# Kernel optimization log

Hardware: AMD Instinct MI355X
Metric: run time of the kernel (lower is better)

The kernel has to match this reference:

```python
import jax, jax.numpy as jnp
import numpy as np

B = 5                      # dat_sz hardcoded in module; kernel shapes force batch == 5
X_DIM = 4096
H_DIM = 4096
T_DIM = 4096
D_DIM = X_DIM // T_DIM     # = 1 (required so z_dim == t_dim broadcasts in reparameterize_nm)
L_DIM = D_DIM * (D_DIM + 1) // 2
Z_DIM = T_DIM * L_DIM      # = 4096


def _linear_params(key, din, dout):
    kw, kb = jax.random.split(key)
    W = jax.random.normal(kw, (din, dout), dtype=jnp.float32) / np.float32(np.sqrt(din))
    b = jax.random.normal(kb, (dout,), dtype=jnp.float32) * np.float32(0.01)
    return W, b


def setup_inputs() -> dict:
    key = jax.random.key(0)
    ks = jax.random.split(key, 20)
    inp = {}
    inp["x"] = jax.random.normal(ks[0], (B, X_DIM), dtype=jnp.float32)
    inp["eps_xi"] = jax.random.normal(ks[1], (B, T_DIM), dtype=jnp.float32)
    inp["eps_f"] = jax.random.normal(ks[2], (B, D_DIM), dtype=jnp.float32)
    inp["eps_z"] = jax.random.normal(ks[3], (B, Z_DIM), dtype=jnp.float32)
    inp["W1"], inp["b1"] = _linear_params(ks[4], X_DIM, H_DIM)
    inp["W11"], inp["b11"] = _linear_params(ks[5], H_DIM, T_DIM)
    inp["W12"], inp["b12"] = _linear_params(ks[6], H_DIM, T_DIM)
    inp["W2"], inp["b2"] = _linear_params(ks[7], D_DIM, H_DIM)
    inp["W21"], inp["b21"] = _linear_params(ks[8], H_DIM, Z_DIM)
    inp["W22"], inp["b22"] = _linear_params(ks[9], H_DIM, T_DIM)
    inp["W23"], inp["b23"] = _linear_params(ks[10], X_DIM + Z_DIM, H_DIM)
    inp["W24"], inp["b24"] = _linear_params(ks[11], H_DIM, T_DIM + D_DIM)
    inp["W25"], inp["b25"] = _linear_params(ks[12], H_DIM, T_DIM + D_DIM)
    inp["W3"], inp["b3"] = _linear_params(ks[13], Z_DIM, H_DIM)
    inp["W31"], inp["b31"] = _linear_params(ks[14], H_DIM, X_DIM)
    inp["W32"], inp["b32"] = _linear_params(ks[15], H_DIM, X_DIM)
    inp["s"] = jax.random.normal(ks[16], (B, T_DIM), dtype=jnp.float32)
    inp["t"] = jax.random.normal(ks[17], (B, D_DIM), dtype=jnp.float32)
    inp["sigma"] = jnp.asarray(0.01, dtype=jnp.float32)
    inp["w"] = jnp.ones((T_DIM,), dtype=jnp.float32) / np.float32(T_DIM)
    inp["dist"] = 1  # unused by forward (matches torch signature)
    return inp


def _ard_kernel(a, b, sigma, w):
    # K[i,j] = sigma^2 * exp(-0.5 * sum_d w_d (a_i,d - b_j,d)^2)
    # Vectorized replacement of the original O(B^2) Python double loop.
    d2 = (a[:, None, :] - b[None, :, :]) ** 2            # [B, B, T]
    return (sigma ** 2) * jnp.exp(-0.5 * jnp.einsum('ijt,t->ij', d2, w))


def reference(x, eps_xi, eps_f, eps_z,
              W1, b1, W11, b11, W12, b12,
              W2, b2, W21, b21, W22, b22,
              W23, b23, W24, b24, W25, b25,
              W3, b3, W31, b31, W32, b32,
              s, t, sigma, w, dist):
    relu = jax.nn.relu
    # encode_1
    h1 = relu(x @ W1 + b1)
    qxi_mean = h1 @ W11 + b11
    log_qxi_cov = h1 @ W12 + b12
    # reparameterize_nm
    xi = jnp.exp(0.5 * log_qxi_cov) * eps_xi + qxi_mean
    # reparameterize_gp (training branch)
    K_ss = _ard_kernel(s, s, sigma, w)                    # [5,5]
    K_xs = _ard_kernel(xi, s, sigma, w)                   # [5,5]
    kk_inv = K_xs @ jnp.linalg.inv(K_ss)                  # [5,5]
    qf_mean = kk_inv @ t                                  # [5,D]
    cov = _ard_kernel(xi, xi, sigma, w) - kk_inv @ _ard_kernel(s, xi, sigma, w)
    qf_cov = jnp.diag(cov)                                # [5]
    f = jnp.sqrt(qf_cov)[:, None] * eps_f + qf_mean       # [5,D]
    # encode_2
    h2 = relu(f @ W2 + b2)
    z_mean = h2 @ W21 + b21                               # [5,Z]
    z_cov = h2 @ W22 + b22                                # [5,T] (== Z since d_dim=1)
    z = jnp.exp(0.5 * z_cov) * eps_z + z_mean
    # encode_3
    h23 = relu(jnp.concatenate([x, z], axis=1) @ W23 + b23)
    r_mean = h23 @ W24 + b24                              # [5,T+D]
    r_cov = h23 @ W25 + b25
    # decode
    h3 = relu(z @ W3 + b3)
    x_mean = h3 @ W31 + b31
    x_cov = h3 @ W32 + b32
    # losses
    qf_cov2 = jnp.broadcast_to(qf_cov[:, None], (B, D_DIM))
    q_mean = jnp.concatenate([qxi_mean, qf_mean], axis=1)
    q_cov = jnp.concatenate([log_qxi_cov, jnp.log(qf_cov2)], axis=1)
    kld1 = 0.5 * jnp.sum(-z_cov - 1.0 + jnp.exp(z_cov) + z_mean ** 2) / B
    kld2 = 0.5 * jnp.sum(r_cov - q_cov - 1.0
                         + jnp.exp(q_cov - r_cov)
                         + (q_mean - r_mean) ** 2 * jnp.exp(-r_cov)) / B
    kld_loss = kld1 + kld2
    log_pi = jnp.log(jnp.asarray(np.pi, dtype=jnp.float32))
    nll_loss = 0.5 * jnp.sum(log_pi + x_cov + jnp.exp(-x_cov) * (x - x_mean) ** 2) / B
    return (kld_loss, nll_loss, z_mean, z_cov, x_mean, x_cov)
```

## Files before the change

kernel.cpp:

```cpp
#include <hip/hip_runtime.h>
#include <math.h>

#define B5 5
#define DX 4096
#define DT 4096
#define DR 4097

enum {
  WS_SUMS  = 0,
  WS_CNT1  = 3,
  WS_CNT2  = 4,
  WS_ZERO_END = 8,
  WS_ACT1  = 16,
  WS_ACT23 = WS_ACT1  + 20480,
  WS_ACT3  = WS_ACT23 + 20480,
  WS_QXI_F = WS_ACT3  + 20480,
  WS_LQC_F = WS_QXI_F + 20480,
  WS_XIV   = WS_LQC_F + 20480,
  WS_Z     = WS_XIV   + 20480,
  WS_KSS   = WS_Z     + 20480,
  WS_KXS   = WS_KSS + 32,
  WS_F     = WS_KXS + 32,
  WS_QFM   = WS_F   + 8,
  WS_QFC   = WS_QFM + 8,
  WS_PART  = 143472,
  WS_P_H1  = WS_PART,
  WS_P_QXI = WS_P_H1  + 1310720,
  WS_P_LQC = WS_P_QXI + 1310720,
  WS_P_ZM  = WS_P_LQC + 1310720,
  WS_P_ZC  = WS_P_ZM  + 1310720,
  WS_P_H23 = WS_P_ZC  + 1310720,
  WS_P_H3  = WS_P_H23 + 2621440,
  WS_P_RM  = WS_P_H3  + 1310720,
  WS_P_RC  = WS_P_RM  + 1311040,
  WS_P_XM  = WS_P_RC  + 1311040,
  WS_P_XC  = WS_P_XM  + 1310720,
  WS_END   = WS_P_XC  + 1310720
};

#define GCOLS 128
#define GK    64
#define WROWS 16

__device__ inline float wave_sum(float v) {
  #pragma unroll
  for (int o = 32; o > 0; o >>= 1) v += __shfl_down(v, o, 64);
  return v;
}

template<int PROLOG, int DUAL, int ALIGNED>
__device__ __forceinline__ void gemm5_body(
    float* sx, float* red, int bx, int by,
    const float* __restrict__ p0, const float* __restrict__ p1,
    const float* __restrict__ p2,
    const float* __restrict__ Wa, const float* __restrict__ Wb,
    float* __restrict__ Pa,       float* __restrict__ Pb,
    int din, int dout)
{
  const int tid  = threadIdx.x;
  const int lane = tid & 63;
  const int wv   = tid >> 6;
  const long i0  = (long)by * GK;
  const long r0  = i0 + (long)wv * WROWS;

  float* sw = sx + wv * 80;
  for (int t = lane; t < B5 * WROWS; t += 64) {
    int b  = t >> 4;
    int il = t & 15;
    int i  = (int)(r0 + il);
    float v;
    if (PROLOG == 0)      v = p0[(long)b * din + i];
    else if (PROLOG == 2) v = fmaxf(p0[b] * p1[i] + p2[i], 0.f);
    else                  v = (i < DX) ? p0[(long)b * DX + i] : p1[(long)b * DT + (i - DX)];
    sw[t] = v;
  }

  const long o0 = (long)bx * GCOLS + lane * 2;
  const bool v0 = (o0 < dout);
  const bool v1 = (o0 + 1 < dout);

  float accA[B5][2] = {};
  float accB[B5][2] = {};
  const float* wa = Wa + r0 * dout + o0;
  const float* wb = DUAL ? (Wb + r0 * dout + o0) : nullptr;

  #pragma unroll 8
  for (int il = 0; il < WROWS; ++il) {
    float w0a, w1a, w0b = 0.f, w1b = 0.f;
    if (ALIGNED) {
      float2 ta = *(const float2*)wa; w0a = ta.x; w1a = ta.y;
      if (DUAL) { float2 tb = *(const float2*)wb; w0b = tb.x; w1b = tb.y; }
    } else {
      w0a = v0 ? wa[0] : 0.f; w1a = v1 ? wa[1] : 0.f;
      if (DUAL) { w0b = v0 ? wb[0] : 0.f; w1b = v1 ? wb[1] : 0.f; }
    }
    #pragma unroll
    for (int b = 0; b < B5; ++b) {
      float xv = sw[b * WROWS + il];
      accA[b][0] += xv * w0a; accA[b][1] += xv * w1a;
      if (DUAL) { accB[b][0] += xv * w0b; accB[b][1] += xv * w1b; }
    }
    wa += dout; if (DUAL) wb += dout;
  }

  const int NJ = DUAL ? 20 : 10;
  if (wv > 0) {
    float* rr = red + (long)(wv - 1) * NJ * 64 + lane;
    #pragma unroll
    for (int b = 0; b < B5; ++b) {
      rr[(b*2)*64] = accA[b][0]; rr[(b*2+1)*64] = accA[b][1];
      if (DUAL) { rr[(10+b*2)*64] = accB[b][0]; rr[(10+b*2+1)*64] = accB[b][1]; }
    }
  }
  __syncthreads();
  if (wv == 0) {
    #pragma unroll
    for (int w2 = 0; w2 < 3; ++w2) {
      const float* rr = red + (long)w2 * NJ * 64 + lane;
      #pragma unroll
      for (int b = 0; b < B5; ++b) {
        accA[b][0] += rr[(b*2)*64]; accA[b][1] += rr[(b*2+1)*64];
        if (DUAL) { accB[b][0] += rr[(10+b*2)*64]; accB[b][1] += rr[(10+b*2+1)*64]; }
      }
    }
    if (v0) {
      #pragma unroll
      for (int b = 0; b < B5; ++b) {
        float* pa = Pa + ((long)by * B5 + b) * dout + o0;
        if (ALIGNED) *(float2*)pa = make_float2(accA[b][0], accA[b][1]);
        else { pa[0] = accA[b][0]; if (v1) pa[1] = accA[b][1]; }
        if (DUAL) {
          float* pb = Pb + ((long)by * B5 + b) * dout + o0;
          if (ALIGNED) *(float2*)pb = make_float2(accB[b][0], accB[b][1]);
          else { pb[0] = accB[b][0]; if (v1) pb[1] = accB[b][1]; }
        }
      }
    }
  }
}

template<int PROLOG, int DUAL, int ALIGNED>
__global__ __launch_bounds__(256) void gemm5(
    const float* __restrict__ p0, const float* __restrict__ p1,
    const float* __restrict__ p2,
    const float* __restrict__ Wa, const float* __restrict__ Wb,
    float* __restrict__ Pa,       float* __restrict__ Pb,
    int din, int dout)
{
  __shared__ float sx[4 * 80];
  __shared__ float red[3 * 20 * 64];
  gemm5_body<PROLOG, DUAL, ALIGNED>(sx, red, blockIdx.x, blockIdx.y,
      p0, p1, p2, Wa, Wb, Pa, Pb, din, dout);
}

__global__ __launch_bounds__(256) void gemm5_G46(
    const float* __restrict__ x,   const float* __restrict__ z,
    const float* __restrict__ W23, float* __restrict__ P23,
    const float* __restrict__ W3,  float* __restrict__ P3)
{
  __shared__ float sx[4 * 80];
  __shared__ float red[3 * 20 * 64];
  int id = blockIdx.x;
  if (id < 4096) {
    gemm5_body<3, 0, 1>(sx, red, id & 31, id >> 5, x, z, nullptr,
                        W23, nullptr, P23, nullptr, 8192, 4096);
  } else {
    id -= 4096;
    gemm5_body<0, 0, 1>(sx, red, id & 31, id >> 5, z, nullptr, nullptr,
                        W3, nullptr, P3, nullptr, 4096, 4096);
  }
}

__global__ __launch_bounds__(256) void gemm5_G57(
    const float* __restrict__ act23,
    const float* __restrict__ W24, const float* __restrict__ W25,
    float* __restrict__ PRM,       float* __restrict__ PRC,
    const float* __restrict__ act3,
    const float* __restrict__ W31, const float* __restrict__ W32,
    float* __restrict__ PXM,       float* __restrict__ PXC)
{
  __shared__ float sx[4 * 80];
  __shared__ float red[3 * 20 * 64];
  int id = blockIdx.x;
  if (id < 2112) {
    gemm5_body<0, 1, 0>(sx, red, id % 33, id / 33, act23, nullptr, nullptr,
                        W24, W25, PRM, PRC, 4096, 4097);
  } else {
    id -= 2112;
    gemm5_body<0, 1, 1>(sx, red, id & 31, id >> 5, act3, nullptr, nullptr,
                        W31, W32, PXM, PXC, 4096, 4096);
  }
}

__global__ __launch_bounds__(256) void k_act1(
    const float* __restrict__ P, const float* __restrict__ bias, float* __restrict__ act,
    float* __restrict__ ctrl)
{
  if (blockIdx.x == 0 && threadIdx.x < WS_ZERO_END) ctrl[threadIdx.x] = 0.f;
  int idx = blockIdx.x * 256 + threadIdx.x;
  int b = idx >> 12, col = idx & (DT - 1);
  const float* pp = P + (long)b * DT + col;
  float s = 0.f;
  #pragma unroll 8
  for (int ks = 0; ks < 64; ++ks) s += pp[(long)ks * (B5 * DT)];
  act[idx] = fmaxf(s + bias[col], 0.f);
}

__global__ __launch_bounds__(256) void k_act23(
    const float* __restrict__ P23, const float* __restrict__ b23, float* __restrict__ act23,
    const float* __restrict__ P3,  const float* __restrict__ b3,  float* __restrict__ act3)
{
  int idx = blockIdx.x * 256 + threadIdx.x;
  if (idx < B5 * DT) {
    int b = idx >> 12, col = idx & (DT - 1);
    const float* pp = P23 + (long)b * DT + col;
    float s = 0.f;
    #pragma unroll 8
    for (int ks = 0; ks < 128; ++ks) s += pp[(long)ks * (B5 * DT)];
    act23[idx] = fmaxf(s + b23[col], 0.f);
  } else {
    int j = idx - B5 * DT;
    int b = j >> 12, col = j & (DT - 1);
    const float* pp = P3 + (long)b * DT + col;
    float s = 0.f;
    #pragma unroll 8
    for (int ks = 0; ks < 64; ++ks) s += pp[(long)ks * (B5 * DT)];
    act3[j] = fmaxf(s + b3[col], 0.f);
  }
}

__global__ __launch_bounds__(256) void k_xi(
    const float* __restrict__ Pq, const float* __restrict__ Pl,
    const float* __restrict__ b11, const float* __restrict__ b12,
    const float* __restrict__ eps_xi,
    float* __restrict__ qf, float* __restrict__ lf, float* __restrict__ xiv)
{
  int idx = blockIdx.x * 256 + threadIdx.x;
  if (idx >= B5 * DT) return;
  int b = idx >> 12, col = idx & (DT - 1);
  const float* pq = Pq + (long)b * DT + col;
  const float* pl = Pl + (long)b * DT + col;
  float sq = 0.f, sl = 0.f;
  #pragma unroll 8
  for (int ks = 0; ks < 64; ++ks) { sq += pq[(long)ks * (B5 * DT)]; sl += pl[(long)ks * (B5 * DT)]; }
  float qm = sq + b11[col];
  float lq = sl + b12[col];
  qf[idx] = qm; lf[idx] = lq;
  xiv[idx] = expf(0.5f * lq) * eps_xi[idx] + qm;
}

__global__ __launch_bounds__(256) void k_ardgp(
    const float* __restrict__ s,    const float* __restrict__ xiv,
    const float* __restrict__ w,    const float* __restrict__ sigma,
    const float* __restrict__ t_in, const float* __restrict__ eps_f,
    float* __restrict__ Kss, float* __restrict__ Kxs, int* __restrict__ cnt,
    float* __restrict__ fv, float* __restrict__ qfm, float* __restrict__ qfc)
{
  const int bid = blockIdx.x;
  const bool xs = (bid >= 25);
  int q = xs ? bid - 25 : bid;
  const int i = q / 5, j = q % 5;
  const float* aa = xs ? (xiv + (long)i * DT) : (s + (long)i * DT);
  const float* bb = s + (long)j * DT;

  float sum = 0.f;
  for (int t = threadIdx.x; t < DT; t += 256) {
    float d = aa[t] - bb[t];
    sum += w[t] * d * d;
  }
  sum = wave_sum(sum);
  __shared__ float red[4];
  int lane = threadIdx.x & 63, wv = threadIdx.x >> 6;
  if (lane == 0) red[wv] = sum;
  __syncthreads();

  if (threadIdx.x == 0) {
    float tot = red[0] + red[1] + red[2] + red[3];
    float sg = sigma[0];
    float K = sg * sg * expf(-0.5f * tot);
    (xs ? Kxs : Kss)[i * 5 + j] = K;
    __threadfence();
    int old = atomicAdd(cnt, 1);
    if (old == 49) {
      __threadfence();
      double M[5][5], Inv[5][5];
      for (int a = 0; a < 5; ++a)
        for (int b = 0; b < 5; ++b) { M[a][b] = Kss[a * 5 + b]; Inv[a][b] = (a == b) ? 1.0 : 0.0; }
      for (int c = 0; c < 5; ++c) {
        int p = c; double best = fabs(M[c][c]);
        for (int r = c + 1; r < 5; ++r) if (fabs(M[r][c]) > best) { best = fabs(M[r][c]); p = r; }
        if (p != c)
          for (int k = 0; k < 5; ++k) {
            double tm = M[c][k]; M[c][k] = M[p][k]; M[p][k] = tm;
            tm = Inv[c][k]; Inv[c][k] = Inv[p][k]; Inv[p][k] = tm;
          }
        double piv = 1.0 / M[c][c];
        for (int k = 0; k < 5; ++k) { M[c][k] *= piv; Inv[c][k] *= piv; }
        for (int r = 0; r < 5; ++r) if (r != c) {
          double m = M[r][c];
          for (int k = 0; k < 5; ++k) { M[r][k] -= m * M[c][k]; Inv[r][k] -= m * Inv[c][k]; }
        }
      }
      double kk[5][5];
      for (int a = 0; a < 5; ++a)
        for (int b = 0; b < 5; ++b) {
          double acc = 0.0;
          for (int k = 0; k < 5; ++k) acc += (double)Kxs[a * 5 + k] * Inv[k][b];
          kk[a][b] = acc;
        }
      double sg2 = (double)sg * (double)sg;
      for (int a = 0; a < 5; ++a) {
        double qm = 0.0, qc = sg2;
        for (int b = 0; b < 5; ++b) { qm += kk[a][b] * (double)t_in[b]; qc -= kk[a][b] * (double)Kxs[a * 5 + b]; }
        if (qc < 1e-12) qc = 1e-12;
        qfm[a] = (float)qm;
        qfc[a] = (float)qc;
        fv[a]  = sqrtf((float)qc) * eps_f[a] + (float)qm;
      }
    }
  }
}

__global__ __launch_bounds__(256) void k_z(
    const float* __restrict__ Pm, const float* __restrict__ Pc,
    const float* __restrict__ b21, const float* __restrict__ b22,
    const float* __restrict__ eps_z,
    float* __restrict__ out_zm, float* __restrict__ out_zc,
    float* __restrict__ zv, float* __restrict__ kld1sum)
{
  int idx = blockIdx.x * 256 + threadIdx.x;
  float term = 0.f;
  if (idx < B5 * DT) {
    int b = idx >> 12, col = idx & (DT - 1);
    const float* pm = Pm + (long)b * DT + col;
    const float* pc = Pc + (long)b * DT + col;
    float sm = 0.f, sc = 0.f;
    #pragma unroll 8
    for (int ks = 0; ks < 64; ++ks) { sm += pm[(long)ks * (B5 * DT)]; sc += pc[(long)ks * (B5 * DT)]; }
    float zm = sm + b21[col];
    float zc = sc + b22[col];
    out_zm[idx] = zm; out_zc[idx] = zc;
    zv[idx] = expf(0.5f * zc) * eps_z[idx] + zm;
    term = -zc - 1.f + expf(zc) + zm * zm;
  }
  term = wave_sum(term);
  if ((threadIdx.x & 63) == 0) atomicAdd(kld1sum, term);
}

__global__ __launch_bounds__(256) void k_fin(
    const float* __restrict__ Prm, const float* __restrict__ Prc,
    const float* __restrict__ b24, const float* __restrict__ b25,
    const float* __restrict__ qxi, const float* __restrict__ lqc,
    const float* __restrict__ qfm, const float* __restrict__ qfc,
    const float* __restrict__ Pxm, const float* __restrict__ Pxc,
    const float* __restrict__ b31, const float* __restrict__ b32,
    const float* __restrict__ x,
    float* __restrict__ out_xm, float* __restrict__ out_xc,
    float* __restrict__ sums, int* __restrict__ cnt, float* __restrict__ out01)
{
  const int gtid = blockIdx.x * 256 + threadIdx.x;
  float t2 = 0.f, t3 = 0.f;
  if (gtid < B5 * DR) {
    int b = gtid / DR, col = gtid % DR;
    const float* pm = Prm + (long)b * DR + col;
    const float* pc = Prc + (long)b * DR + col;
    float sm = 0.f, sc = 0.f;
    #pragma unroll 8
    for (int ks = 0; ks < 64; ++ks) { sm += pm[(long)ks * (B5 * DR)]; sc += pc[(long)ks * (B5 * DR)]; }
    float rm = sm + b24[col];
    float rc = sc + b25[col];
    float qm, qc;
    if (col < DT) { qm = qxi[(long)b * DT + col]; qc = lqc[(long)b * DT + col]; }
    else          { qm = qfm[b]; qc = logf(qfc[b]); }
    float d = qm - rm;
    t2 = rc - qc - 1.f + expf(qc - rc) + d * d * expf(-rc);
  } else {
    int idx = gtid - B5 * DR;
    if (idx < B5 * DX) {
      int b = idx >> 12, col = idx & (DX - 1);
      const float* pm = Pxm + (long)b * DX + col;
      const float* pc = Pxc + (long)b * DX + col;
      float sm = 0.f, sc = 0.f;
      #pragma unroll 8
      for (int ks = 0; ks < 64; ++ks) { sm += pm[(long)ks * (B5 * DX)]; sc += pc[(long)ks * (B5 * DX)]; }
      float xm = sm + b31[col];
      float xc = sc + b32[col];
      out_xm[idx] = xm; out_xc[idx] = xc;
      float d = x[idx] - xm;
      t3 = 1.14472988584940017f + xc + expf(-xc) * d * d;
    }
  }
  t2 = wave_sum(t2);
  t3 = wave_sum(t3);
  if ((threadIdx.x & 63) == 0) {
    if (t2 != 0.f) atomicAdd(&sums[1], t2);
    if (t3 != 0.f) atomicAdd(&sums[2], t3);
  }
  __syncthreads();
  if (threadIdx.x == 0) {
    __threadfence();
    int old = atomicAdd(cnt, 1);
    if (old == (int)gridDim.x - 1) {
      __threadfence();
      out01[0] = 0.5f * (sums[0] + sums[1]) / (float)B5;
      out01[1] = 0.5f * sums[2] / (float)B5;
    }
  }
}

extern "C" void kernel_launch(void* const* d_in, const int* in_sizes, int n_in,
                              void* d_out, int out_size, void* d_ws, size_t ws_size,
                              hipStream_t stream)
{
  const float* x      = (const float*)d_in[0];
  const float* eps_xi = (const float*)d_in[1];
  const float* eps_f  = (const float*)d_in[2];
  const float* eps_z  = (const float*)d_in[3];
  const float* W1  = (const float*)d_in[4];  const float* b1  = (const float*)d_in[5];
  const float* W11 = (const float*)d_in[6];  const float* b11 = (const float*)d_in[7];
  const float* W12 = (const float*)d_in[8];  const float* b12 = (const float*)d_in[9];
  const float* W2  = (const float*)d_in[10]; const float* b2  = (const float*)d_in[11];
  const float* W21 = (const float*)d_in[12]; const float* b21 = (const float*)d_in[13];
  const float* W22 = (const float*)d_in[14]; const float* b22 = (const float*)d_in[15];
  const float* W23 = (const float*)d_in[16]; const float* b23 = (const float*)d_in[17];
  const float* W24 = (const float*)d_in[18]; const float* b24 = (const float*)d_in[19];
  const float* W25 = (const float*)d_in[20]; const float* b25 = (const float*)d_in[21];
  const float* W3  = (const float*)d_in[22]; const float* b3  = (const float*)d_in[23];
  const float* W31 = (const float*)d_in[24]; const float* b31 = (const float*)d_in[25];
  const float* W32 = (const float*)d_in[26]; const float* b32 = (const float*)d_in[27];
  const float* s     = (const float*)d_in[28];
  const float* t     = (const float*)d_in[29];
  const float* sigma = (const float*)d_in[30];
  const float* w     = (const float*)d_in[31];

  float* ws  = (float*)d_ws;
  float* out = (float*)d_out;

  dim3 blk(256);

  gemm5<0,0,1><<<dim3(32,64), blk, 0, stream>>>(
      x, nullptr, nullptr, W1, nullptr, ws + WS_P_H1, nullptr, 4096, 4096);
  k_act1<<<80, blk, 0, stream>>>(ws + WS_P_H1, b1, ws + WS_ACT1, ws);
  gemm5<0,1,1><<<dim3(32,64), blk, 0, stream>>>(
      ws + WS_ACT1, nullptr, nullptr, W11, W12, ws + WS_P_QXI, ws + WS_P_LQC, 4096, 4096);
  k_xi<<<80, blk, 0, stream>>>(
      ws + WS_P_QXI, ws + WS_P_LQC, b11, b12, eps_xi,
      ws + WS_QXI_F, ws + WS_LQC_F, ws + WS_XIV);
  k_ardgp<<<50, blk, 0, stream>>>(
      s, ws + WS_XIV, w, sigma, t, eps_f,
      ws + WS_KSS, ws + WS_KXS, (int*)(ws + WS_CNT1),
      ws + WS_F, ws + WS_QFM, ws + WS_QFC);
  gemm5<2,1,1><<<dim3(32,64), blk, 0, stream>>>(
      ws + WS_F, W2, b2, W21, W22, ws + WS_P_ZM, ws + WS_P_ZC, 4096, 4096);
  k_z<<<80, blk, 0, stream>>>(
      ws + WS_P_ZM, ws + WS_P_ZC, b21, b22, eps_z,
      out + 2, out + 2 + 20480, ws + WS_Z, ws + WS_SUMS);
  gemm5_G46<<<6144, blk, 0, stream>>>(
      x, ws + WS_Z, W23, ws + WS_P_H23, W3, ws + WS_P_H3);
  k_act23<<<160, blk, 0, stream>>>(
      ws + WS_P_H23, b23, ws + WS_ACT23, ws + WS_P_H3, b3, ws + WS_ACT3);
  gemm5_G57<<<4160, blk, 0, stream>>>(
      ws + WS_ACT23, W24, W25, ws + WS_P_RM, ws + WS_P_RC,
      ws + WS_ACT3,  W31, W32, ws + WS_P_XM, ws + WS_P_XC);
  k_fin<<<161, blk, 0, stream>>>(
      ws + WS_P_RM, ws + WS_P_RC, b24, b25,
      ws + WS_QXI_F, ws + WS_LQC_F,
      ws + WS_QFM, ws + WS_QFC,
      ws + WS_P_XM, ws + WS_P_XC, b31, b32, x,
      out + 2 + 40960, out + 2 + 61440,
      ws + WS_SUMS, (int*)(ws + WS_CNT2), out);
}
```

Baseline: 242.0 us.

## Split-K partial reductions across 8 warps per block and fuse xi with ARD kernel

```diff
diff --git a/kernel.cpp b/kernel.cpp
--- a/kernel.cpp
+++ b/kernel.cpp
@@ -5,11 +5,14 @@
 #define DX 4096
 #define DT 4096
 #define DR 4097
+#define PSZ 20480
+#define PSZR 20485
 
 enum {
   WS_SUMS  = 0,
-  WS_CNT1  = 3,
-  WS_CNT2  = 4,
+  WS_CNT_XI  = 3,
+  WS_CNT_FIN = 4,
+  WS_CNT_ARD = 5,
   WS_ZERO_END = 8,
   WS_ACT1  = 16,
   WS_ACT23 = WS_ACT1  + 20480,
@@ -48,6 +51,26 @@
   return v;
 }
 
+template<int PER>
+__device__ __forceinline__ float red_block(
+    const float* __restrict__ P, long psz, long e, int tid, float* r)
+{
+  int j = tid >> 5;
+  const float* pp = P + (long)j * PER * psz + e;
+  float s = 0.f;
+  #pragma unroll
+  for (int k = 0; k < PER; ++k) s += pp[(long)k * psz];
+  r[tid] = s;
+  __syncthreads();
+  float tot = 0.f;
+  if (tid < 32) {
+    #pragma unroll
+    for (int jj = 0; jj < 8; ++jj) tot += r[jj * 32 + tid];
+  }
+  __syncthreads();
+  return tot;
+}
+
 template<int PROLOG, int DUAL, int ALIGNED>
 __device__ __forceinline__ void gemm5_body(
     float* sx, float* red, int bx, int by,
@@ -197,90 +220,101 @@
     float* __restrict__ ctrl)
 {
   if (blockIdx.x == 0 && threadIdx.x < WS_ZERO_END) ctrl[threadIdx.x] = 0.f;
-  int idx = blockIdx.x * 256 + threadIdx.x;
-  int b = idx >> 12, col = idx & (DT - 1);
-  const float* pp = P + (long)b * DT + col;
-  float s = 0.f;
-  #pragma unroll 8
-  for (int ks = 0; ks < 64; ++ks) s += pp[(long)ks * (B5 * DT)];
-  act[idx] = fmaxf(s + bias[col], 0.f);
+  __shared__ float r[256];
+  int tid = threadIdx.x;
+  long e = (long)blockIdx.x * 32 + (tid & 31);
+  float s = red_block<8>(P, PSZ, e, tid, r);
+  if (tid < 32) {
+    int col = (int)(e & 4095);
+    act[e] = fmaxf(s + bias[col], 0.f);
+  }
 }
 
 __global__ __launch_bounds__(256) void k_act23(
     const float* __restrict__ P23, const float* __restrict__ b23, float* __restrict__ act23,
     const float* __restrict__ P3,  const float* __restrict__ b3,  float* __restrict__ act3)
 {
-  int idx = blockIdx.x * 256 + threadIdx.x;
-  if (idx < B5 * DT) {
-    int b = idx >> 12, col = idx & (DT - 1);
-    const float* pp = P23 + (long)b * DT + col;
-    float s = 0.f;
-    #pragma unroll 8
-    for (int ks = 0; ks < 128; ++ks) s += pp[(long)ks * (B5 * DT)];
-    act23[idx] = fmaxf(s + b23[col], 0.f);
+  __shared__ float r[256];
+  int tid = threadIdx.x;
+  if (blockIdx.x < 640) {
+    long e = (long)blockIdx.x * 32 + (tid & 31);
+    float s = red_block<16>(P23, PSZ, e, tid, r);
+    if (tid < 32) {
+      int col = (int)(e & 4095);
+      act23[e] = fmaxf(s + b23[col], 0.f);
+    }
   } else {
-    int j = idx - B5 * DT;
-    int b = j >> 12, col = j & (DT - 1);
-    const float* pp = P3 + (long)b * DT + col;
-    float s = 0.f;
-    #pragma unroll 8
-    for (int ks = 0; ks < 64; ++ks) s += pp[(long)ks * (B5 * DT)];
-    act3[j] = fmaxf(s + b3[col], 0.f);
-  }
-}
-
-__global__ __launch_bounds__(256) void k_xi(
+    long e = (long)(blockIdx.x - 640) * 32 + (tid & 31);
+    float s = red_block<8>(P3, PSZ, e, tid, r);
+    if (tid < 32) {
+      int col = (int)(e & 4095);
+      act3[e] = fmaxf(s + b3[col], 0.f);
+    }
+  }
+}
+
+__global__ __launch_bounds__(256) void k_xiard(
     const float* __restrict__ Pq, const float* __restrict__ Pl,
     const float* __restrict__ b11, const float* __restrict__ b12,
     const float* __restrict__ eps_xi,
-    float* __restrict__ qf, float* __restrict__ lf, float* __restrict__ xiv)
-{
-  int idx = blockIdx.x * 256 + threadIdx.x;
-  if (idx >= B5 * DT) return;
-  int b = idx >> 12, col = idx & (DT - 1);
-  const float* pq = Pq + (long)b * DT + col;
-  const float* pl = Pl + (long)b * DT + col;
-  float sq = 0.f, sl = 0.f;
-  #pragma unroll 8
-  for (int ks = 0; ks < 64; ++ks) { sq += pq[(long)ks * (B5 * DT)]; sl += pl[(long)ks * (B5 * DT)]; }
-  float qm = sq + b11[col];
-  float lq = sl + b12[col];
-  qf[idx] = qm; lf[idx] = lq;
-  xiv[idx] = expf(0.5f * lq) * eps_xi[idx] + qm;
-}
-
-__global__ __launch_bounds__(256) void k_ardgp(
-    const float* __restrict__ s,    const float* __restrict__ xiv,
-    const float* __restrict__ w,    const float* __restrict__ sigma,
+    const float* __restrict__ s,   const float* __restrict__ w,
+    const float* __restrict__ sigma,
     const float* __restrict__ t_in, const float* __restrict__ eps_f,
-    float* __restrict__ Kss, float* __restrict__ Kxs, int* __restrict__ cnt,
+    float* __restrict__ qf, float* __restrict__ lf, float* __restrict__ xiv,
+    float* __restrict__ Kss, float* __restrict__ Kxs,
+    int* __restrict__ cnt_xi, int* __restrict__ cnt_ard,
     float* __restrict__ fv, float* __restrict__ qfm, float* __restrict__ qfc)
 {
-  const int bid = blockIdx.x;
+  __shared__ float r[256];
+  int tid = threadIdx.x;
+  if (blockIdx.x < 640) {
+    long e = (long)blockIdx.x * 32 + (tid & 31);
+    float sq = red_block<8>(Pq, PSZ, e, tid, r);
+    float sl = red_block<8>(Pl, PSZ, e, tid, r);
+    if (tid < 32) {
+      int col = (int)(e & 4095);
+      float qm = sq + b11[col];
+      float lq = sl + b12[col];
+      qf[e] = qm; lf[e] = lq;
+      xiv[e] = expf(0.5f * lq) * eps_xi[e] + qm;
+    }
+    __threadfence();
+    __syncthreads();
+    if (tid == 0) atomicAdd(cnt_xi, 1);
+    return;
+  }
+
+  const int bid = blockIdx.x - 640;
   const bool xs = (bid >= 25);
   int q = xs ? bid - 25 : bid;
   const int i = q / 5, j = q % 5;
+
+  if (xs) {
+    if (tid == 0) { while (atomicAdd(cnt_xi, 0) < 640) {} }
+    __syncthreads();
+    __threadfence();
+  }
   const float* aa = xs ? (xiv + (long)i * DT) : (s + (long)i * DT);
   const float* bb = s + (long)j * DT;
 
   float sum = 0.f;
-  for (int t = threadIdx.x; t < DT; t += 256) {
+  for (int t = tid; t < DT; t += 256) {
     float d = aa[t] - bb[t];
     sum += w[t] * d * d;
   }
   sum = wave_sum(sum);
-  __shared__ float red[4];
-  int lane = threadIdx.x & 63, wv = threadIdx.x >> 6;
-  if (lane == 0) red[wv] = sum;
+  __shared__ float red4[4];
+  int lane = tid & 63, wv = tid >> 6;
+  if (lane == 0) red4[wv] = sum;
   __syncthreads();
 
-  if (threadIdx.x == 0) {
-    float tot = red[0] + red[1] + red[2] + red[3];
+  if (tid == 0) {
+    float tot = red4[0] + red4[1] + red4[2] + red4[3];
     float sg = sigma[0];
     float K = sg * sg * expf(-0.5f * tot);
     (xs ? Kxs : Kss)[i * 5 + j] = K;
     __threadfence();
-    int old = atomicAdd(cnt, 1);
+    int old = atomicAdd(cnt_ard, 1);
     if (old == 49) {
       __threadfence();
       double M[5][5], Inv[5][5];
@@ -288,7 +322,7 @@
         for (int b = 0; b < 5; ++b) { M[a][b] = Kss[a * 5 + b]; Inv[a][b] = (a == b) ? 1.0 : 0.0; }
       for (int c = 0; c < 5; ++c) {
         int p = c; double best = fabs(M[c][c]);
-        for (int r = c + 1; r < 5; ++r) if (fabs(M[r][c]) > best) { best = fabs(M[r][c]); p = r; }
+        for (int rr = c + 1; rr < 5; ++rr) if (fabs(M[rr][c]) > best) { best = fabs(M[rr][c]); p = rr; }
         if (p != c)
           for (int k = 0; k < 5; ++k) {
             double tm = M[c][k]; M[c][k] = M[p][k]; M[p][k] = tm;
@@ -296,9 +330,9 @@
           }
         double piv = 1.0 / M[c][c];
         for (int k = 0; k < 5; ++k) { M[c][k] *= piv; Inv[c][k] *= piv; }
-        for (int r = 0; r < 5; ++r) if (r != c) {
-          double m = M[r][c];
-          for (int k = 0; k < 5; ++k) { M[r][k] -= m * M[c][k]; Inv[r][k] -= m * Inv[c][k]; }
+        for (int rr = 0; rr < 5; ++rr) if (rr != c) {
+          double m = M[rr][c];
+          for (int k = 0; k < 5; ++k) { M[rr][k] -= m * M[c][k]; Inv[rr][k] -= m * Inv[c][k]; }
         }
       }
       double kk[5][5];
@@ -328,23 +362,24 @@
     float* __restrict__ out_zm, float* __restrict__ out_zc,
     float* __restrict__ zv, float* __restrict__ kld1sum)
 {
-  int idx = blockIdx.x * 256 + threadIdx.x;
+  __shared__ float r[256];
+  int tid = threadIdx.x;
+  long e = (long)blockIdx.x * 32 + (tid & 31);
+  float sm = red_block<8>(Pm, PSZ, e, tid, r);
+  float sc = red_block<8>(Pc, PSZ, e, tid, r);
   float term = 0.f;
-  if (idx < B5 * DT) {
-    int b = idx >> 12, col = idx & (DT - 1);
-    const float* pm = Pm + (long)b * DT + col;
-    const float* pc = Pc + (long)b * DT + col;
-    float sm = 0.f, sc = 0.f;
-    #pragma unroll 8
-    for (int ks = 0; ks < 64; ++ks) { sm += pm[(long)ks * (B5 * DT)]; sc += pc[(long)ks * (B5 * DT)]; }
+  if (tid < 32) {
+    int col = (int)(e & 4095);
     float zm = sm + b21[col];
     float zc = sc + b22[col];
-    out_zm[idx] = zm; out_zc[idx] = zc;
-    zv[idx] = expf(0.5f * zc) * eps_z[idx] + zm;
+    out_zm[e] = zm; out_zc[e] = zc;
+    zv[e] = expf(0.5f * zc) * eps_z[e] + zm;
     term = -zc - 1.f + expf(zc) + zm * zm;
   }
-  term = wave_sum(term);
-  if ((threadIdx.x & 63) == 0) atomicAdd(kld1sum, term);
+  if (tid < 64) {
+    term = wave_sum(term);
+    if (tid == 0 && term != 0.f) atomicAdd(kld1sum, term);
+  }
 }
 
 __global__ __launch_bounds__(256) void k_fin(
@@ -358,46 +393,49 @@
     float* __restrict__ out_xm, float* __restrict__ out_xc,
     float* __restrict__ sums, int* __restrict__ cnt, float* __restrict__ out01)
 {
-  const int gtid = blockIdx.x * 256 + threadIdx.x;
-  float t2 = 0.f, t3 = 0.f;
-  if (gtid < B5 * DR) {
-    int b = gtid / DR, col = gtid % DR;
-    const float* pm = Prm + (long)b * DR + col;
-    const float* pc = Prc + (long)b * DR + col;
-    float sm = 0.f, sc = 0.f;
-    #pragma unroll 8
-    for (int ks = 0; ks < 64; ++ks) { sm += pm[(long)ks * (B5 * DR)]; sc += pc[(long)ks * (B5 * DR)]; }
-    float rm = sm + b24[col];
-    float rc = sc + b25[col];
-    float qm, qc;
-    if (col < DT) { qm = qxi[(long)b * DT + col]; qc = lqc[(long)b * DT + col]; }
-    else          { qm = qfm[b]; qc = logf(qfc[b]); }
-    float d = qm - rm;
-    t2 = rc - qc - 1.f + expf(qc - rc) + d * d * expf(-rc);
+  __shared__ float r[256];
+  int tid = threadIdx.x;
+  if (blockIdx.x < 641) {
+    long e = (long)blockIdx.x * 32 + (tid & 31);
+    bool valid = (e < B5 * DR);
+    long ec = valid ? e : (B5 * DR - 1);
+    float sm = red_block<8>(Prm, PSZR, ec, tid, r);
+    float sc = red_block<8>(Prc, PSZR, ec, tid, r);
+    float t2 = 0.f;
+    if (tid < 32 && valid) {
+      int b = (int)(e / DR), col = (int)(e % DR);
+      float rm = sm + b24[col];
+      float rc = sc + b25[col];
+      float qm, qc;
+      if (col < DT) { qm = qxi[(long)b * DT + col]; qc = lqc[(long)b * DT + col]; }
+      else          { qm = qfm[b]; qc = logf(qfc[b]); }
+      float d = qm - rm;
+      t2 = rc - qc - 1.f + expf(qc - rc) + d * d * expf(-rc);
+    }
+    if (tid < 64) {
+      t2 = wave_sum(t2);
+      if (tid == 0 && t2 != 0.f) atomicAdd(&sums[1], t2);
+    }
   } else {
-    int idx = gtid - B5 * DR;
-    if (idx < B5 * DX) {
-      int b = idx >> 12, col = idx & (DX - 1);
-      const float* pm = Pxm + (long)b * DX + col;
-      const float* pc = Pxc + (long)b * DX + col;
-      float sm = 0.f, sc = 0.f;
-      #pragma unroll 8
-      for (int ks = 0; ks < 64; ++ks) { sm += pm[(long)ks * (B5 * DX)]; sc += pc[(long)ks * (B5 * DX)]; }
+    long e = (long)(blockIdx.x - 641) * 32 + (tid & 31);
+    float sm = red_block<8>(Pxm, PSZ, e, tid, r);
+    float sc = red_block<8>(Pxc, PSZ, e, tid, r);
+    float t3 = 0.f;
+    if (tid < 32) {
+      int col = (int)(e & 4095);
       float xm = sm + b31[col];
       float xc = sc + b32[col];
-      out_xm[idx] = xm; out_xc[idx] = xc;
-      float d = x[idx] - xm;
+      out_xm[e] = xm; out_xc[e] = xc;
+      float d = x[e] - xm;
       t3 = 1.14472988584940017f + xc + expf(-xc) * d * d;
     }
-  }
-  t2 = wave_sum(t2);
-  t3 = wave_sum(t3);
-  if ((threadIdx.x & 63) == 0) {
-    if (t2 != 0.f) atomicAdd(&sums[1], t2);
-    if (t3 != 0.f) atomicAdd(&sums[2], t3);
+    if (tid < 64) {
+      t3 = wave_sum(t3);
+      if (tid == 0 && t3 != 0.f) atomicAdd(&sums[2], t3);
+    }
   }
   __syncthreads();
-  if (threadIdx.x == 0) {
+  if (tid == 0) {
     __threadfence();
     int old = atomicAdd(cnt, 1);
     if (old == (int)gridDim.x - 1) {
@@ -440,33 +478,33 @@
 
   gemm5<0,0,1><<<dim3(32,64), blk, 0, stream>>>(
       x, nullptr, nullptr, W1, nullptr, ws + WS_P_H1, nullptr, 4096, 4096);
-  k_act1<<<80, blk, 0, stream>>>(ws + WS_P_H1, b1, ws + WS_ACT1, ws);
+  k_act1<<<640, blk, 0, stream>>>(ws + WS_P_H1, b1, ws + WS_ACT1, ws);
   gemm5<0,1,1><<<dim3(32,64), blk, 0, stream>>>(
       ws + WS_ACT1, nullptr, nullptr, W11, W12, ws + WS_P_QXI, ws + WS_P_LQC, 4096, 4096);
-  k_xi<<<80, blk, 0, stream>>>(
+  k_xiard<<<690, blk, 0, stream>>>(
       ws + WS_P_QXI, ws + WS_P_LQC, b11, b12, eps_xi,
-      ws + WS_QXI_F, ws + WS_LQC_F, ws + WS_XIV);
-  k_ardgp<<<50, blk, 0, stream>>>(
-      s, ws + WS_XIV, w, sigma, t, eps_f,
-      ws + WS_KSS, ws + WS_KXS, (int*)(ws + WS_CNT1),
+      s, w, sigma, t, eps_f,
+      ws + WS_QXI_F, ws + WS_LQC_F, ws + WS_XIV,
+      ws + WS_KSS, ws + WS_KXS,
+      (int*)(ws + WS_CNT_XI), (int*)(ws + WS_CNT_ARD),
       ws + WS_F, ws + WS_QFM, ws + WS_QFC);
   gemm5<2,1,1><<<dim3(32,64), blk, 0, stream>>>(
       ws + WS_F, W2, b2, W21, W22, ws + WS_P_ZM, ws + WS_P_ZC, 4096, 4096);
-  k_z<<<80, blk, 0, stream>>>(
+  k_z<<<640, blk, 0, stream>>>(
       ws + WS_P_ZM, ws + WS_P_ZC, b21, b22, eps_z,
       out + 2, out + 2 + 20480, ws + WS_Z, ws + WS_SUMS);
   gemm5_G46<<<6144, blk, 0, stream>>>(
       x, ws + WS_Z, W23, ws + WS_P_H23, W3, ws + WS_P_H3);
-  k_act23<<<160, blk, 0, stream>>>(
+  k_act23<<<1280, blk, 0, stream>>>(
       ws + WS_P_H23, b23, ws + WS_ACT23, ws + WS_P_H3, b3, ws + WS_ACT3);
   gemm5_G57<<<4160, blk, 0, stream>>>(
       ws + WS_ACT23, W24, W25, ws + WS_P_RM, ws + WS_P_RC,
       ws + WS_ACT3,  W31, W32, ws + WS_P_XM, ws + WS_P_XC);
-  k_fin<<<161, blk, 0, stream>>>(
+  k_fin<<<1281, blk, 0, stream>>>(
       ws + WS_P_RM, ws + WS_P_RC, b24, b25,
       ws + WS_QXI_F, ws + WS_LQC_F,
       ws + WS_QFM, ws + WS_QFC,
       ws + WS_P_XM, ws + WS_P_XC, b31, b32, x,
       out + 2 + 40960, out + 2 + 61440,
-      ws + WS_SUMS, (int*)(ws + WS_CNT2), out);
-}
+      ws + WS_SUMS, (int*)(ws + WS_CNT_FIN), out);
+}
```

Measured after the change: 305.3 us. +26.2%, slower.
